# Performance work log

Hardware: AMD Instinct MI355X
Metric: run time of the kernel (lower is better)

The kernel has to match this reference:

```python
import jax, jax.numpy as jnp
import numpy as np

B, T, E, D, N, L, NF = 4, 2048, 512, 512, 16, 4, 2048


def setup_inputs() -> dict:
    key = jax.random.key(0)
    ks = jax.random.split(key, 12)
    r = lambda k, s, sc=1.0: jax.random.normal(k, s, dtype=jnp.float32) * sc
    return {
        "text_emb": r(ks[0], (B, T, E)),
        "W_in": r(ks[1], (E, D), 1.0 / np.sqrt(E).astype(np.float32)),
        "b_in": jnp.zeros((D,), jnp.float32),
        "freq_pe": r(ks[2], (NF, D), 0.02),
        # diagonal-SSM (S4D) params per layer, stacked on leading L axis
        "A_log": r(ks[3], (L, D, N), 0.5),
        "B_ssm": r(ks[4], (L, D, N), 0.5),
        "C_ssm": r(ks[5], (L, D, N), 0.5),
        "log_dt": r(ks[6], (L, D), 0.5) - 4.6,  # dt ~ 0.01
        "D_skip": r(ks[7], (L, D), 0.5),
        "ln_f0_scale": jnp.ones((D,), jnp.float32),
        "ln_f0_bias": jnp.zeros((D,), jnp.float32),
        "W_f0": r(ks[8], (D, 1), 1.0 / np.sqrt(D).astype(np.float32)),
        "b_f0": jnp.zeros((1,), jnp.float32),
        "ln_en_scale": jnp.ones((D,), jnp.float32),
        "ln_en_bias": jnp.zeros((D,), jnp.float32),
        "W_en": r(ks[9], (D, 1), 1.0 / np.sqrt(D).astype(np.float32)),
        "b_en": jnp.zeros((1,), jnp.float32),
    }


def _layernorm(x, scale, bias, eps=1e-5):
    mu = jnp.mean(x, axis=-1, keepdims=True)
    var = jnp.mean(jnp.square(x - mu), axis=-1, keepdims=True)
    return (x - mu) * jax.lax.rsqrt(var + eps) * scale + bias


def _s4_layer(h, A_log, Bm, Cm, log_dt, Dsk):
    # h: [B, T, D]; diagonal SSM with ZOH discretization, scanned over T.
    dt = jnp.exp(log_dt)                 # [D]
    A = -jnp.exp(A_log)                  # [D, N], stable (negative real)
    Abar = jnp.exp(dt[:, None] * A)      # [D, N]
    Bbar = (Abar - 1.0) / A * Bm         # [D, N]
    u_t = jnp.transpose(h, (1, 0, 2))    # [T, B, D]
    x0 = jnp.zeros((h.shape[0], h.shape[2], A.shape[1]), h.dtype)  # [B, D, N]

    def step(x, u):
        x = Abar * x + Bbar * u[..., None]          # [B, D, N]
        y = jnp.einsum('bdn,dn->bd', x, Cm)         # readout
        return x, y

    _, ys = jax.lax.scan(step, x0, u_t)             # ys: [T, B, D]
    y = jnp.transpose(ys, (1, 0, 2)) + Dsk * h      # D skip connection
    return h + jax.nn.gelu(y)                       # residual + activation


def _forward(text_emb, W_in, b_in, freq_pe, A_log, B_ssm, C_ssm, log_dt,
             D_skip, ln_f0_scale, ln_f0_bias, W_f0, b_f0,
             ln_en_scale, ln_en_bias, W_en, b_en):
    x = text_emb @ W_in + b_in                      # [B, T, D]
    Tlen = x.shape[1]
    nf = freq_pe.shape[0]
    if nf >= Tlen:                                  # static-shape crop
        freq = freq_pe[:Tlen]
    else:                                           # static-shape edge pad
        pad = jnp.repeat(freq_pe[-1:], Tlen - nf, axis=0)
        freq = jnp.concatenate([freq_pe, pad], axis=0)
    h = x + freq[None, :, :]
    for l in range(A_log.shape[0]):
        h = _s4_layer(h, A_log[l], B_ssm[l], C_ssm[l], log_dt[l], D_skip[l])
    f0 = (_layernorm(h, ln_f0_scale, ln_f0_bias) @ W_f0 + b_f0)[..., 0]
    en = (_layernorm(h, ln_en_scale, ln_en_bias) @ W_en + b_en)[..., 0]
    return f0, en


def reference(text_emb, W_in, b_in, freq_pe, A_log, B_ssm, C_ssm, log_dt,
              D_skip, ln_f0_scale, ln_f0_bias, W_f0, b_f0,
              ln_en_scale, ln_en_bias, W_en, b_en):
    return _forward(text_emb, W_in, b_in, freq_pe, A_log, B_ssm, C_ssm,
                    log_dt, D_skip, ln_f0_scale, ln_f0_bias, W_f0, b_f0,
                    ln_en_scale, ln_en_bias, W_en, b_en)
```

## Files before the change

kernel.cpp:

```cpp
#include <hip/hip_runtime.h>

#define B_   4
#define T_   2048
#define E_   512
#define D_   512
#define N_   16
#define L_   4
#define TCH  32
#define ROWS_PB 4

typedef __bf16 bf16x8 __attribute__((ext_vector_type(8)));
typedef float  f32x4  __attribute__((ext_vector_type(4)));
typedef float  f32x2  __attribute__((ext_vector_type(2)));
typedef unsigned short us8 __attribute__((ext_vector_type(8)));

__device__ __forceinline__ float us2f(unsigned short u) {
    return __uint_as_float(((unsigned int)u) << 16);
}
__device__ __forceinline__ unsigned short f2us(float f) {
    unsigned int u = __float_as_uint(f);
    unsigned int r = (u + 0x7fffu + ((u >> 16) & 1u)) >> 16;
    return (unsigned short)r;
}
__device__ __forceinline__ float ldin(const void* p, int i, unsigned int f) {
    return f ? ((const float*)p)[i] : us2f(((const unsigned short*)p)[i]);
}
__device__ __forceinline__ unsigned int probe_f32(const void* lnfs) {
    return (((const unsigned int*)lnfs)[0] == 0x3F800000u) ? 1u : 0u;
}
__device__ __forceinline__ f32x2 pk_fma(f32x2 a, f32x2 b, f32x2 c) {
    f32x2 d;
    asm("v_pk_fma_f32 %0, %1, %2, %3" : "=v"(d) : "v"(a), "v"(b), "v"(c));
    return d;
}
__device__ __forceinline__ f32x2 pk_mul(f32x2 a, f32x2 b) {
    f32x2 d;
    asm("v_pk_mul_f32 %0, %1, %2" : "=v"(d) : "v"(a), "v"(b));
    return d;
}

#define PA    0
#define PB    32768
#define PC    65536
#define PDT   98304
#define PDSK  100352
#define PLFS  102400
#define PLFB  102912
#define PWF   103424
#define PLES  103936
#define PLEB  104448
#define PWEN  104960
#define PSC   105472
#define PRM_N 105474

#define NB_TEXT 2048
#define NB_PRM  413
#define NB_WT   64
#define NB_S4P  128

__global__ __launch_bounds__(256) void prep_kernel(
    const void* X, const void* Win,
    const void* A_log, const void* B_ssm, const void* C_ssm,
    const void* log_dt, const void* D_skip,
    const void* lnfs, const void* lnfb, const void* Wf0,
    const void* lnes, const void* lneb, const void* Wen,
    const void* bf0, const void* ben,
    unsigned short* __restrict__ textc, unsigned short* __restrict__ Wt,
    float* __restrict__ P, float* __restrict__ P2) {
    __shared__ float tile[64 * 65];
    unsigned int f = probe_f32(lnfs);
    int bid = blockIdx.x;
    if (bid < NB_TEXT) {
        int i = (bid * 256 + threadIdx.x) * 8;
        if (f) {
            const float* xf = (const float*)X;
            us8 r;
#pragma unroll
            for (int j = 0; j < 8; j++) r[j] = f2us(xf[i + j]);
            *(us8*)(textc + i) = r;
        } else {
            *(us8*)(textc + i) = *(const us8*)((const unsigned short*)X + i);
        }
    } else if (bid < NB_TEXT + NB_PRM) {
        int i = (bid - NB_TEXT) * 256 + threadIdx.x;
        if      (i < PB)     P[i] = ldin(A_log,  i - PA,   f);
        else if (i < PC)     P[i] = ldin(B_ssm,  i - PB,   f);
        else if (i < PDT)    P[i] = ldin(C_ssm,  i - PC,   f);
        else if (i < PDSK)   P[i] = ldin(log_dt, i - PDT,  f);
        else if (i < PLFS)   P[i] = ldin(D_skip, i - PDSK, f);
        else if (i < PLFB)   P[i] = ldin(lnfs,   i - PLFS, f);
        else if (i < PWF)    P[i] = ldin(lnfb,   i - PLFB, f);
        else if (i < PLES)   P[i] = ldin(Wf0,    i - PWF,  f);
        else if (i < PLEB)   P[i] = ldin(lnes,   i - PLES, f);
        else if (i < PWEN)   P[i] = ldin(lneb,   i - PLEB, f);
        else if (i < PSC)    P[i] = ldin(Wen,    i - PWEN, f);
        else if (i == PSC)     P[i] = ldin(bf0, 0, f);
        else if (i == PSC + 1) P[i] = ldin(ben, 0, f);
    } else if (bid < NB_TEXT + NB_PRM + NB_WT) {
        int tb = bid - (NB_TEXT + NB_PRM);
        int d0 = (tb >> 3) * 64, e0 = (tb & 7) * 64;
        int r = threadIdx.x >> 6, i = threadIdx.x & 63;
#pragma unroll
        for (int k = 0; k < 16; k++) {
            int e = k * 4 + r;
            tile[e * 65 + i] = ldin(Win, (e0 + e) * D_ + d0 + i, f);
        }
        __syncthreads();
#pragma unroll
        for (int k = 0; k < 16; k++) {
            int dd = k * 4 + r;
            Wt[(size_t)(d0 + dd) * E_ + e0 + i] = f2us(tile[i * 65 + dd]);
        }
    } else {
        int i = (bid - (NB_TEXT + NB_PRM + NB_WT)) * 256 + threadIdx.x;
        int n = i & 15;
        int ld = i >> 4;
        float dt = __expf(ldin(log_dt, ld, f));
        float A  = -__expf(ldin(A_log, i, f));
        float Ab = __expf(dt * A);
        float Bb = (Ab - 1.f) / A * ldin(B_ssm, i, f);
        float m  = Ab * Ab;
        m = m * m; m = m * m; m = m * m; m = m * m;
        int base = ld * 64 + n;
        P2[base]      = Ab;
        P2[base + 16] = Bb;
        P2[base + 32] = ldin(C_ssm, i, f);
        P2[base + 48] = m;
    }
}

__global__ __launch_bounds__(256) void gemm_kernel(const unsigned short* __restrict__ X,
                                                   const unsigned short* __restrict__ Wt,
                                                   const void* __restrict__ freq,
                                                   const void* __restrict__ b_in,
                                                   const void* __restrict__ lnfs,
                                                   float* __restrict__ H) {
    __shared__ unsigned short wlds[64 * 264];
    const unsigned int fl = probe_f32(lnfs);
    const int tid = threadIdx.x;
    const int w  = tid >> 6;
    const int ln = tid & 15;
    const int q  = (tid >> 4) & 3;
    const int d0 = blockIdx.x * 64;
    const int t0 = blockIdx.y * 128;
    const int b  = blockIdx.z;

    f32x4 acc[2][4];
#pragma unroll
    for (int i = 0; i < 2; i++)
#pragma unroll
        for (int j = 0; j < 4; j++) { acc[i][j][0]=0.f; acc[i][j][1]=0.f; acc[i][j][2]=0.f; acc[i][j][3]=0.f; }

    const size_t xbase = ((size_t)b * T_ + t0) * E_;

#pragma unroll
    for (int p = 0; p < 2; ++p) {
        if (p) __syncthreads();
#pragma unroll
        for (int it = 0; it < 8; ++it) {
            int flat = it * 256 + tid;
            int d = flat >> 5;
            int e = (flat & 31) << 3;
            bf16x8 v = *(const bf16x8*)(Wt + (size_t)(d0 + d) * E_ + p * 256 + e);
            *(bf16x8*)(wlds + d * 264 + e) = v;
        }
        __syncthreads();
#pragma unroll
        for (int s = 0; s < 8; ++s) {
            const int eo = s * 32 + q * 8;
            bf16x8 bfr[4];
#pragma unroll
            for (int j = 0; j < 4; j++)
                bfr[j] = *(const bf16x8*)(wlds + (j * 16 + ln) * 264 + eo);
#pragma unroll
            for (int sub = 0; sub < 2; ++sub) {
                const int t = w * 32 + sub * 16 + ln;
                bf16x8 afr = *(const bf16x8*)(X + xbase + (size_t)t * E_ + p * 256 + eo);
#pragma unroll
                for (int j = 0; j < 4; j++)
                    acc[sub][j] = __builtin_amdgcn_mfma_f32_16x16x32_bf16(afr, bfr[j], acc[sub][j], 0, 0, 0);
            }
        }
    }
#pragma unroll
    for (int sub = 0; sub < 2; ++sub) {
#pragma unroll
        for (int j = 0; j < 4; j++) {
            int d  = d0 + j * 16 + ln;
            int tb = t0 + w * 32 + sub * 16 + q * 4;
            float bi = ldin(b_in, d, fl);
            f32x4 o;
#pragma unroll
            for (int r4 = 0; r4 < 4; r4++)
                o[r4] = acc[sub][j][r4] + ldin(freq, (tb + r4) * D_ + d, fl) + bi;
            *(f32x4*)(H + ((size_t)b * D_ + d) * T_ + tb) = o;
        }
    }
}

__global__ __launch_bounds__(256) __attribute__((amdgpu_waves_per_eu(2, 2)))
void s4_kernel(float* __restrict__ H, const float* __restrict__ P,
               const float* __restrict__ P2) {
    __shared__ float xl[ROWS_PB][64 * 33];
    const int w = threadIdx.x >> 6, lane = threadIdx.x & 63;
    const int row = blockIdx.x * ROWS_PB + w;
    const int d = row & (D_ - 1);
    float* Xw  = xl[w];
    float* Xme = Xw + lane * 33;
    float* gp  = H + (size_t)row * T_;

#pragma unroll
    for (int k = 0; k < 8; k++) {
        int idx = k * 256 + lane * 4;
        f32x4 v = *(const f32x4*)(gp + idx);
        int s = (idx >> 5) * 33 + (idx & 31);
        Xw[s] = v[0]; Xw[s + 1] = v[1]; Xw[s + 2] = v[2]; Xw[s + 3] = v[3];
    }
    __syncthreads();

    for (int l = 0; l < L_; ++l) {
        const float* pp = P2 + (size_t)(((l << 9) + d) << 6);
        float Dsk = P[PDSK + l * D_ + d];
        f32x2 Ab[8], Bb[8], Cc[8], M[8];
#pragma unroll
        for (int n = 0; n < 8; n++) {
            Ab[n] = *(const f32x2*)(pp + 2 * n);
            Bb[n] = *(const f32x2*)(pp + 16 + 2 * n);
            Cc[n] = *(const f32x2*)(pp + 32 + 2 * n);
            M[n]  = *(const f32x2*)(pp + 48 + 2 * n);
        }
        f32x2 b[8];
#pragma unroll
        for (int n = 0; n < 8; n++) { b[n][0] = 0.f; b[n][1] = 0.f; }
#pragma unroll 4
        for (int j = 0; j < TCH; j++) {
            float uu = Xme[j];
            f32x2 u2; u2[0] = uu; u2[1] = uu;
#pragma unroll
            for (int n = 0; n < 8; n++) b[n] = pk_fma(Ab[n], b[n], pk_mul(Bb[n], u2));
        }
#pragma unroll
        for (int dd = 1; dd < 64; dd <<= 1) {
            bool g = lane >= dd;
#pragma unroll
            for (int n = 0; n < 8; n++) {
                f32x2 bp;
                bp[0] = __shfl_up(b[n][0], (unsigned)dd, 64);
                bp[1] = __shfl_up(b[n][1], (unsigned)dd, 64);
                if (g) b[n] = pk_fma(M[n], bp, b[n]);
            }
            if (dd < 32) {
#pragma unroll
                for (int n = 0; n < 8; n++) M[n] = pk_mul(M[n], M[n]);
            }
        }
        f32x2 x[8];
#pragma unroll
        for (int n = 0; n < 8; n++) {
            x[n][0] = __shfl_up(b[n][0], 1u, 64);
            x[n][1] = __shfl_up(b[n][1], 1u, 64);
            if (lane == 0) { x[n][0] = 0.f; x[n][1] = 0.f; }
        }
#pragma unroll 4
        for (int j = 0; j < TCH; j++) {
            float uu = Xme[j];
            f32x2 u2; u2[0] = uu; u2[1] = uu;
#pragma unroll
            for (int n = 0; n < 8; n++) x[n] = pk_fma(Ab[n], x[n], pk_mul(Bb[n], u2));
            f32x2 ya; ya[0] = 0.f; ya[1] = 0.f;
            f32x2 yb; yb[0] = 0.f; yb[1] = 0.f;
#pragma unroll
            for (int n = 0; n < 8; n += 2) {
                ya = pk_fma(x[n], Cc[n], ya);
                yb = pk_fma(x[n + 1], Cc[n + 1], yb);
            }
            float y = (ya[0] + yb[0]) + (ya[1] + yb[1]);
            y = fmaf(Dsk, uu, y);
            float zin = 0.7978845608028654f * fmaf(0.044715f, y * y * y, y);
            float e2  = __expf(2.f * zin);
            float r   = __builtin_amdgcn_rcpf(e2 + 1.f);
            Xme[j] = (uu + y) - y * r;
        }
    }
    __syncthreads();
#pragma unroll
    for (int k = 0; k < 8; k++) {
        int idx = k * 256 + lane * 4;
        int s = (idx >> 5) * 33 + (idx & 31);
        f32x4 v; v[0] = Xw[s]; v[1] = Xw[s + 1]; v[2] = Xw[s + 2]; v[3] = Xw[s + 3];
        *(f32x4*)(gp + idx) = v;
    }
}

__global__ __launch_bounds__(256) void final_kernel(const float* __restrict__ H,
                                                    const float* __restrict__ P,
                                                    void* __restrict__ out,
                                                    const void* __restrict__ lnfs_raw) {
    __shared__ float red[4][8][64];
    unsigned int f = probe_f32(lnfs_raw);
    int tid = threadIdx.x;
    int w = tid >> 6, tl = tid & 63;
    int tg = blockIdx.x * 64 + tl;
    int b = tg >> 11, t = tg & (T_ - 1);
    float S1=0.f,S2=0.f,Pf=0.f,Pe=0.f,Cf=0.f,Ce=0.f,Df=0.f,De=0.f;
    const float* hp = H + ((size_t)b * D_) * T_ + t;
#pragma unroll 4
    for (int i = 0; i < 128; i++) {
        int d = w * 128 + i;
        float hv = hp[(size_t)d * T_];
        float sf = P[PLFS + d], bfv = P[PLFB + d], wf = P[PWF + d];
        float se = P[PLES + d], bev = P[PLEB + d], we = P[PWEN + d];
        S1 += hv; S2 = fmaf(hv, hv, S2);
        float tf = sf * wf, te = se * we;
        Pf = fmaf(hv, tf, Pf); Pe = fmaf(hv, te, Pe);
        Cf += tf; Ce += te;
        Df = fmaf(bfv, wf, Df); De = fmaf(bev, we, De);
    }
    red[w][0][tl]=S1; red[w][1][tl]=S2; red[w][2][tl]=Pf; red[w][3][tl]=Pe;
    red[w][4][tl]=Cf; red[w][5][tl]=Ce; red[w][6][tl]=Df; red[w][7][tl]=De;
    __syncthreads();
    if (w == 0) {
        float a[8];
#pragma unroll
        for (int k = 0; k < 8; k++)
            a[k] = red[0][k][tl] + red[1][k][tl] + red[2][k][tl] + red[3][k][tl];
        float mu  = a[0] * (1.f / 512.f);
        float var = a[1] * (1.f / 512.f) - mu * mu;
        float r   = rsqrtf(var + 1e-5f);
        float f0  = r * (a[2] - mu * a[4]) + a[6] + P[PSC + 0];
        float en  = r * (a[3] - mu * a[5]) + a[7] + P[PSC + 1];
        if (f) {
            ((float*)out)[tg]           = f0;
            ((float*)out)[B_ * T_ + tg] = en;
        } else {
            ((unsigned short*)out)[tg]           = f2us(f0);
            ((unsigned short*)out)[B_ * T_ + tg] = f2us(en);
        }
    }
}

extern "C" void kernel_launch(void* const* d_in, const int* in_sizes, int n_in,
                              void* d_out, int out_size, void* d_ws, size_t ws_size,
                              hipStream_t stream) {
    (void)in_sizes; (void)n_in; (void)out_size; (void)ws_size;
    float* ws = (float*)d_ws;
    float* P     = ws;
    float* H     = ws + 105504;
    unsigned short* textc = (unsigned short*)(ws + 4299808);
    unsigned short* Wt    = (unsigned short*)(ws + 6396960);
    float* P2    = ws + 6528032;

    prep_kernel<<<dim3(NB_TEXT + NB_PRM + NB_WT + NB_S4P), dim3(256), 0, stream>>>(
        d_in[0], d_in[1], d_in[4], d_in[5], d_in[6], d_in[7], d_in[8],
        d_in[9], d_in[10], d_in[11], d_in[13], d_in[14], d_in[15],
        d_in[12], d_in[16], textc, Wt, P, P2);
    gemm_kernel<<<dim3(8, 16, 4), dim3(256), 0, stream>>>(textc, Wt, d_in[3], d_in[2], d_in[9], H);
    s4_kernel<<<dim3(512), dim3(256), 0, stream>>>(H, P, P2);
    final_kernel<<<dim3(128), dim3(256), 0, stream>>>(H, P, d_out, d_in[9]);
}
```

Baseline: 191.4 us.

## Fold C into B, use DPP scan with closed-form decay powers, transpose LDS

The S4 scan folds C into Bbar, so each lane carries C-weighted states and the readout becomes a plain sum over n instead of a multiply-accumulate. The cross-lane prefix scan moves from __shfl_up (ds_bpermute) to DPP row_shr and row_bcast steps. The cross-row decay factors are computed directly as exp2 of a precomputed log2, replacing repeated squaring of a stored power. The LDS staging layout is transposed so lanes read consecutive addresses, and the block-wide syncthreads are dropped because each wave only touches its own slice. The risks are exactness of the DPP bound-control and bank-mask semantics, plus the numerical change from computing decay powers with exp2.

```diff
diff --git a/kernel.cpp b/kernel.cpp
--- a/kernel.cpp
+++ b/kernel.cpp
@@ -8,6 +8,7 @@
 #define L_   4
 #define TCH  32
 #define ROWS_PB 4
+#define US_  65
 
 typedef __bf16 bf16x8 __attribute__((ext_vector_type(8)));
 typedef float  f32x4  __attribute__((ext_vector_type(4)));
@@ -37,6 +38,13 @@
     f32x2 d;
     asm("v_pk_mul_f32 %0, %1, %2" : "=v"(d) : "v"(a), "v"(b));
     return d;
+}
+template<int CTRL, int RM>
+__device__ __forceinline__ f32x2 dpp2(f32x2 v) {
+    f32x2 r;
+    r[0] = __int_as_float(__builtin_amdgcn_update_dpp(0, __float_as_int(v[0]), CTRL, RM, 0xF, true));
+    r[1] = __int_as_float(__builtin_amdgcn_update_dpp(0, __float_as_int(v[1]), CTRL, RM, 0xF, true));
+    return r;
 }
 
 #define PA    0
@@ -119,13 +127,12 @@
         float A  = -__expf(ldin(A_log, i, f));
         float Ab = __expf(dt * A);
         float Bb = (Ab - 1.f) / A * ldin(B_ssm, i, f);
-        float m  = Ab * Ab;
-        m = m * m; m = m * m; m = m * m; m = m * m;
+        float l2M = 46.166241308446828f * dt * A;
         int base = ld * 64 + n;
         P2[base]      = Ab;
-        P2[base + 16] = Bb;
-        P2[base + 32] = ldin(C_ssm, i, f);
-        P2[base + 48] = m;
+        P2[base + 16] = Bb * ldin(C_ssm, i, f);
+        P2[base + 32] = exp2f(l2M);
+        P2[base + 48] = l2M;
     }
 }
 
@@ -201,94 +208,109 @@
 __global__ __launch_bounds__(256) __attribute__((amdgpu_waves_per_eu(2, 2)))
 void s4_kernel(float* __restrict__ H, const float* __restrict__ P,
                const float* __restrict__ P2) {
-    __shared__ float xl[ROWS_PB][64 * 33];
+    __shared__ float xl[ROWS_PB][TCH * US_];
     const int w = threadIdx.x >> 6, lane = threadIdx.x & 63;
     const int row = blockIdx.x * ROWS_PB + w;
     const int d = row & (D_ - 1);
     float* Xw  = xl[w];
-    float* Xme = Xw + lane * 33;
+    float* Xme = Xw + lane;
     float* gp  = H + (size_t)row * T_;
 
 #pragma unroll
     for (int k = 0; k < 8; k++) {
-        int idx = k * 256 + lane * 4;
-        f32x4 v = *(const f32x4*)(gp + idx);
-        int s = (idx >> 5) * 33 + (idx & 31);
-        Xw[s] = v[0]; Xw[s + 1] = v[1]; Xw[s + 2] = v[2]; Xw[s + 3] = v[3];
-    }
-    __syncthreads();
+        int m = k * 256 + lane * 4;
+        f32x4 v = *(const f32x4*)(gp + m);
+#pragma unroll
+        for (int i = 0; i < 4; i++) {
+            int t = m + i;
+            Xw[(t & 31) * US_ + (t >> 5)] = v[i];
+        }
+    }
 
     for (int l = 0; l < L_; ++l) {
         const float* pp = P2 + (size_t)(((l << 9) + d) << 6);
         float Dsk = P[PDSK + l * D_ + d];
-        f32x2 Ab[8], Bb[8], Cc[8], M[8];
+        f32x2 Ab[8], CB[8];
 #pragma unroll
         for (int n = 0; n < 8; n++) {
             Ab[n] = *(const f32x2*)(pp + 2 * n);
-            Bb[n] = *(const f32x2*)(pp + 16 + 2 * n);
-            Cc[n] = *(const f32x2*)(pp + 32 + 2 * n);
-            M[n]  = *(const f32x2*)(pp + 48 + 2 * n);
+            CB[n] = *(const f32x2*)(pp + 16 + 2 * n);
         }
         f32x2 b[8];
 #pragma unroll
         for (int n = 0; n < 8; n++) { b[n][0] = 0.f; b[n][1] = 0.f; }
-#pragma unroll 4
+#pragma unroll 8
         for (int j = 0; j < TCH; j++) {
-            float uu = Xme[j];
+            float uu = Xme[j * US_];
             f32x2 u2; u2[0] = uu; u2[1] = uu;
 #pragma unroll
-            for (int n = 0; n < 8; n++) b[n] = pk_fma(Ab[n], b[n], pk_mul(Bb[n], u2));
-        }
-#pragma unroll
-        for (int dd = 1; dd < 64; dd <<= 1) {
-            bool g = lane >= dd;
+            for (int n = 0; n < 8; n++) b[n] = pk_fma(Ab[n], b[n], pk_mul(CB[n], u2));
+        }
+        {
+            f32x2 M1[8], w1[8], w2[8];
+            float e1 = (float)((lane & 15) + 1);
+            float e2l = (float)((lane & 31) + 1);
 #pragma unroll
             for (int n = 0; n < 8; n++) {
-                f32x2 bp;
-                bp[0] = __shfl_up(b[n][0], (unsigned)dd, 64);
-                bp[1] = __shfl_up(b[n][1], (unsigned)dd, 64);
-                if (g) b[n] = pk_fma(M[n], bp, b[n]);
+                M1[n] = *(const f32x2*)(pp + 32 + 2 * n);
+                f32x2 l2m = *(const f32x2*)(pp + 48 + 2 * n);
+                w1[n][0] = exp2f(l2m[0] * e1);  w1[n][1] = exp2f(l2m[1] * e1);
+                w2[n][0] = exp2f(l2m[0] * e2l); w2[n][1] = exp2f(l2m[1] * e2l);
             }
-            if (dd < 32) {
-#pragma unroll
-                for (int n = 0; n < 8; n++) M[n] = pk_mul(M[n], M[n]);
-            }
-        }
-        f32x2 x[8];
+#pragma unroll
+            for (int n = 0; n < 8; n++) b[n] = pk_fma(M1[n], dpp2<0x111, 0xF>(b[n]), b[n]);
+#pragma unroll
+            for (int n = 0; n < 8; n++) M1[n] = pk_mul(M1[n], M1[n]);
+#pragma unroll
+            for (int n = 0; n < 8; n++) b[n] = pk_fma(M1[n], dpp2<0x112, 0xF>(b[n]), b[n]);
+#pragma unroll
+            for (int n = 0; n < 8; n++) M1[n] = pk_mul(M1[n], M1[n]);
+#pragma unroll
+            for (int n = 0; n < 8; n++) b[n] = pk_fma(M1[n], dpp2<0x114, 0xF>(b[n]), b[n]);
+#pragma unroll
+            for (int n = 0; n < 8; n++) M1[n] = pk_mul(M1[n], M1[n]);
+#pragma unroll
+            for (int n = 0; n < 8; n++) b[n] = pk_fma(M1[n], dpp2<0x118, 0xF>(b[n]), b[n]);
+#pragma unroll
+            for (int n = 0; n < 8; n++) b[n] = pk_fma(w1[n], dpp2<0x142, 0xA>(b[n]), b[n]);
+#pragma unroll
+            for (int n = 0; n < 8; n++) b[n] = pk_fma(w2[n], dpp2<0x143, 0xC>(b[n]), b[n]);
+        }
+        f32x2 z[8];
 #pragma unroll
         for (int n = 0; n < 8; n++) {
-            x[n][0] = __shfl_up(b[n][0], 1u, 64);
-            x[n][1] = __shfl_up(b[n][1], 1u, 64);
-            if (lane == 0) { x[n][0] = 0.f; x[n][1] = 0.f; }
-        }
-#pragma unroll 4
+            z[n][0] = __shfl_up(b[n][0], 1u, 64);
+            z[n][1] = __shfl_up(b[n][1], 1u, 64);
+            if (lane == 0) { z[n][0] = 0.f; z[n][1] = 0.f; }
+        }
+#pragma unroll 8
         for (int j = 0; j < TCH; j++) {
-            float uu = Xme[j];
+            float uu = Xme[j * US_];
             f32x2 u2; u2[0] = uu; u2[1] = uu;
 #pragma unroll
-            for (int n = 0; n < 8; n++) x[n] = pk_fma(Ab[n], x[n], pk_mul(Bb[n], u2));
-            f32x2 ya; ya[0] = 0.f; ya[1] = 0.f;
-            f32x2 yb; yb[0] = 0.f; yb[1] = 0.f;
-#pragma unroll
-            for (int n = 0; n < 8; n += 2) {
-                ya = pk_fma(x[n], Cc[n], ya);
-                yb = pk_fma(x[n + 1], Cc[n + 1], yb);
-            }
-            float y = (ya[0] + yb[0]) + (ya[1] + yb[1]);
-            y = fmaf(Dsk, uu, y);
+            for (int n = 0; n < 8; n++) z[n] = pk_fma(Ab[n], z[n], pk_mul(CB[n], u2));
+            f32x2 s0 = z[0] + z[1];
+            f32x2 s1 = z[2] + z[3];
+            f32x2 s2 = z[4] + z[5];
+            f32x2 s3 = z[6] + z[7];
+            s0 = (s0 + s1) + (s2 + s3);
+            float y = fmaf(Dsk, uu, s0[0] + s0[1]);
             float zin = 0.7978845608028654f * fmaf(0.044715f, y * y * y, y);
             float e2  = __expf(2.f * zin);
             float r   = __builtin_amdgcn_rcpf(e2 + 1.f);
-            Xme[j] = (uu + y) - y * r;
-        }
-    }
-    __syncthreads();
+            Xme[j * US_] = (uu + y) - y * r;
+        }
+    }
 #pragma unroll
     for (int k = 0; k < 8; k++) {
-        int idx = k * 256 + lane * 4;
-        int s = (idx >> 5) * 33 + (idx & 31);
-        f32x4 v; v[0] = Xw[s]; v[1] = Xw[s + 1]; v[2] = Xw[s + 2]; v[3] = Xw[s + 3];
-        *(f32x4*)(gp + idx) = v;
+        int m = k * 256 + lane * 4;
+        f32x4 v;
+#pragma unroll
+        for (int i = 0; i < 4; i++) {
+            int t = m + i;
+            v[i] = Xw[(t & 31) * US_ + (t >> 5)];
+        }
+        *(f32x4*)(gp + m) = v;
     }
 }
 
```

Measured after the change: 176.8 us. 1.08x faster.
